# Kernel tuning notes

Hardware: AMD Instinct MI355X
Metric: run time of the kernel (lower is better)

## Reference

```python
import jax, jax.numpy as jnp
import numpy as np

NUM_C = 1000
DIM_S = 128
SIZE_M = 64
B = 64
L = 512


def setup_inputs() -> dict:
    key = jax.random.key(0)
    ks = jax.random.split(key, 16)
    d = DIM_S
    inp = {
        "q": jax.random.randint(ks[0], (B, L), 0, NUM_C),
        "r": jax.random.randint(ks[1], (B, L), 0, 2),
        # embeddings
        "Ek": jax.random.normal(ks[2], (NUM_C, d), jnp.float32),
        "Ev": jax.random.normal(ks[3], (2 * NUM_C, d), jnp.float32),
        # memory key / initial value memory (kaiming-normal-ish)
        "Mk": jax.random.normal(ks[4], (SIZE_M, d), jnp.float32) * np.sqrt(2.0 / d),
        "Mv0": jax.random.normal(ks[5], (SIZE_M, d), jnp.float32) * np.sqrt(2.0 / d),
        # erase / add layers (d -> d)
        "We": jax.random.normal(ks[6], (d, d), jnp.float32) / np.sqrt(d),
        "be": jnp.zeros((d,), jnp.float32),
        "Wa": jax.random.normal(ks[7], (d, d), jnp.float32) / np.sqrt(d),
        "ba": jnp.zeros((d,), jnp.float32),
        # f layer (2d -> d)
        "Wf": jax.random.normal(ks[8], (2 * d, d), jnp.float32) / np.sqrt(2 * d),
        "bf": jnp.zeros((d,), jnp.float32),
        # p layer (d -> 1)
        "Wp": jax.random.normal(ks[9], (d, 1), jnp.float32) / np.sqrt(d),
        "bp": jnp.zeros((1,), jnp.float32),
    }
    return inp


def reference(q, r, Ek, Ev, Mk, Mv0, We, be, Wa, ba, Wf, bf, Wp, bp):
    # q, r: [B, L] int
    x = q + NUM_C * r
    k = Ek[q]            # [B, L, D]  (k_original; no extra features when use_ed=use_mp=0)
    v = Ev[x]            # [B, L, D]

    # correlation weights over memory slots
    w = jax.nn.softmax(jnp.einsum("bld,md->blm", k, Mk), axis=-1)  # [B, L, M]

    e = jax.nn.sigmoid(v @ We + be)  # [B, L, D] erase
    a = jnp.tanh(v @ Wa + ba)        # [B, L, D] add

    def step(Mvt, inputs):
        wt, et, at = inputs            # [B,M], [B,D], [B,D]
        # read from memory BEFORE the update (matches Mv[:, :-1] in torch)
        read = jnp.einsum("bm,bmd->bd", wt, Mvt)
        Mvt_new = Mvt * (1.0 - wt[:, :, None] * et[:, None, :]) + wt[:, :, None] * at[:, None, :]
        return Mvt_new, read

    Mv_init = jnp.broadcast_to(Mv0[None], (q.shape[0], SIZE_M, DIM_S))
    xs = (jnp.swapaxes(w, 0, 1), jnp.swapaxes(e, 0, 1), jnp.swapaxes(a, 0, 1))
    _, reads = jax.lax.scan(step, Mv_init, xs)      # reads: [L, B, D]
    read_content = jnp.swapaxes(reads, 0, 1)        # [B, L, D]

    f = jnp.tanh(jnp.concatenate([read_content, k], axis=-1) @ Wf + bf)  # [B, L, D]
    # dropout in eval mode -> identity
    p = jax.nn.sigmoid(f @ Wp + bp)[..., 0]         # [B, L]
    return p
```

## Files before the change

### kernel.cpp

```cpp
#include <hip/hip_runtime.h>
#include <hip/hip_bf16.h>

#define NUM_C 1000
#define DIM   128
#define MM    64
#define BB    64
#define LL    512
#define NROWS (BB * LL)

typedef unsigned short u16;
typedef unsigned int   u32;
typedef short bfrag __attribute__((ext_vector_type(8)));
typedef float f32x4 __attribute__((ext_vector_type(4)));

__device__ __forceinline__ float sigmoidf_fast(float x) { return 1.f / (1.f + __expf(-x)); }
__device__ __forceinline__ float tanhf_fast(float x) { return 1.f - 2.f / (__expf(2.f * x) + 1.f); }

__device__ __forceinline__ u16 f2bf(float x) {
    u32 u = __float_as_uint(x);
    return (u16)((u + 0x7FFFu + ((u >> 16) & 1u)) >> 16);
}
__device__ __forceinline__ float bf2f(u16 h) { return __uint_as_float(((u32)h) << 16); }

__device__ __forceinline__ float quad_swap1(float x) {
    return __int_as_float(__builtin_amdgcn_mov_dpp(__float_as_int(x), 0xB1, 0xF, 0xF, true));
}
__device__ __forceinline__ float quad_swap2(float x) {
    return __int_as_float(__builtin_amdgcn_mov_dpp(__float_as_int(x), 0x4E, 0xF, 0xF, true));
}
__device__ __forceinline__ float row_ror4(float x) {
    return __int_as_float(__builtin_amdgcn_mov_dpp(__float_as_int(x), 0x124, 0xF, 0xF, true));
}
__device__ __forceinline__ float row_ror8(float x) {
    return __int_as_float(__builtin_amdgcn_mov_dpp(__float_as_int(x), 0x128, 0xF, 0xF, true));
}

__device__ __forceinline__ void ld16(const void* g, void* l) {
    __builtin_amdgcn_global_load_lds(
        (const __attribute__((address_space(1))) unsigned int*)g,
        (__attribute__((address_space(3))) unsigned int*)l, 16, 0, 0);
}

__global__ __launch_bounds__(256) void kP(const float* __restrict__ We,
                                          const float* __restrict__ Wa,
                                          const float* __restrict__ Wf,
                                          const float* __restrict__ Mk,
                                          const float* __restrict__ Ek,
                                          const float* __restrict__ Ev,
                                          u16* weT_hi, u16* weT_lo,
                                          u16* waT_hi, u16* waT_lo,
                                          u16* wfT_hi, u16* wfT_lo,
                                          u16* mkT_hi, u16* mkT_lo,
                                          u16* ekbf, u16* evbf) {
    int idx = blockIdx.x * 256 + threadIdx.x;
    if (idx < 128 * 128) {
        int n = idx >> 7, k = idx & 127;
        float we = We[k * DIM + n];
        u16 h = f2bf(we);
        weT_hi[idx] = h; weT_lo[idx] = f2bf(we - bf2f(h));
        float wa = Wa[k * DIM + n];
        u16 h2 = f2bf(wa);
        waT_hi[idx] = h2; waT_lo[idx] = f2bf(wa - bf2f(h2));
    }
    if (idx < 64 * 128) {
        float mk = Mk[idx];
        u16 h = f2bf(mk);
        mkT_hi[idx] = h; mkT_lo[idx] = f2bf(mk - bf2f(h));
    }
    {
        int n = idx >> 8, k = idx & 255;
        float wf = Wf[k * DIM + n];
        u16 h = f2bf(wf);
        wfT_hi[idx] = h; wfT_lo[idx] = f2bf(wf - bf2f(h));
    }
    for (int i = idx; i < NUM_C * DIM; i += 32768) ekbf[i] = f2bf(Ek[i]);
    for (int i = idx; i < 2 * NUM_C * DIM; i += 32768) evbf[i] = f2bf(Ev[i]);
}

__global__ __launch_bounds__(256) void kAB(const int* __restrict__ q,
                                           const int* __restrict__ r,
                                           const u16* __restrict__ ekbf,
                                           const u16* __restrict__ evbf,
                                           const u16* __restrict__ mkT_hi, const u16* __restrict__ mkT_lo,
                                           const u16* __restrict__ weT_hi, const u16* __restrict__ weT_lo,
                                           const u16* __restrict__ waT_hi, const u16* __restrict__ waT_lo,
                                           const float* __restrict__ be, const float* __restrict__ ba,
                                           float* __restrict__ w_out,
                                           float2* __restrict__ ea_out) {
    __shared__ __align__(16) u16 shi[4][16][136];
    __shared__ float slab[4][64];
    const int tid = threadIdx.x;
    const int lane = tid & 63;
    const int wv = tid >> 6;
    const int nloc = lane & 15;
    const int quad = lane >> 4;

    if (blockIdx.x < 512) {
        const int base = blockIdx.x * 64;
        {
            const int row_l = tid >> 2;
            const int rts = row_l >> 4, ms = row_l & 15;
            const int d0 = (tid & 3) * 32;
            const u16* src = ekbf + (size_t)q[base + row_l] * DIM + d0;
            #pragma unroll
            for (int c8 = 0; c8 < 4; ++c8)
                *reinterpret_cast<bfrag*>(&shi[rts][ms][d0 + c8 * 8]) =
                    *reinterpret_cast<const bfrag*>(src + c8 * 8);
        }
        __syncthreads();

        const int n = wv * 16 + nloc;
        bfrag Bh[4], Bl[4];
        #pragma unroll
        for (int kc = 0; kc < 4; ++kc) {
            const int ko = kc * 32 + quad * 8;
            Bh[kc] = *reinterpret_cast<const bfrag*>(mkT_hi + n * DIM + ko);
            Bl[kc] = *reinterpret_cast<const bfrag*>(mkT_lo + n * DIM + ko);
        }

        f32x4 acc[4];
        #pragma unroll
        for (int t = 0; t < 4; ++t) acc[t] = 0.f;

        #pragma unroll
        for (int rt = 0; rt < 4; ++rt) {
            #pragma unroll
            for (int kc = 0; kc < 4; ++kc) {
                const int ko = kc * 32 + quad * 8;
                bfrag Ah = *reinterpret_cast<const bfrag*>(&shi[rt][nloc][ko]);
                acc[rt] = __builtin_amdgcn_mfma_f32_16x16x32_bf16(Ah, Bh[kc], acc[rt], 0, 0, 0);
                acc[rt] = __builtin_amdgcn_mfma_f32_16x16x32_bf16(Ah, Bl[kc], acc[rt], 0, 0, 0);
            }
        }

        float ex[4][4];
        #pragma unroll
        for (int rt = 0; rt < 4; ++rt) {
            #pragma unroll
            for (int rg = 0; rg < 4; ++rg) {
                float e = __expf(acc[rt][rg]);
                ex[rt][rg] = e;
                float s = e;
                s += __shfl_xor(s, 1);
                s += __shfl_xor(s, 2);
                s += __shfl_xor(s, 4);
                s += __shfl_xor(s, 8);
                if (nloc == 0) slab[wv][rt * 16 + quad * 4 + rg] = s;
            }
        }
        __syncthreads();

        #pragma unroll
        for (int rt = 0; rt < 4; ++rt) {
            #pragma unroll
            for (int rg = 0; rg < 4; ++rg) {
                const int row = rt * 16 + quad * 4 + rg;
                float tot = slab[0][row] + slab[1][row] + slab[2][row] + slab[3][row];
                w_out[(size_t)(base + row) * MM + n] = ex[rt][rg] / tot;
            }
        }
    } else {
        const int base = (blockIdx.x - 512) * 64;
        {
            const int row_l = tid >> 2;
            const int rts = row_l >> 4, ms = row_l & 15;
            const int d0 = (tid & 3) * 32;
            const int row = base + row_l;
            const int x = q[row] + NUM_C * r[row];
            const u16* src = evbf + (size_t)x * DIM + d0;
            #pragma unroll
            for (int c8 = 0; c8 < 4; ++c8)
                *reinterpret_cast<bfrag*>(&shi[rts][ms][d0 + c8 * 8]) =
                    *reinterpret_cast<const bfrag*>(src + c8 * 8);
        }
        __syncthreads();

        #pragma unroll
        for (int dt = 0; dt < 2; ++dt) {
            const int n = (wv * 2 + dt) * 16 + nloc;
            bfrag Beh[4], Bel[4], Bah[4], Bal[4];
            #pragma unroll
            for (int kc = 0; kc < 4; ++kc) {
                const int ko = kc * 32 + quad * 8;
                Beh[kc] = *reinterpret_cast<const bfrag*>(weT_hi + n * DIM + ko);
                Bel[kc] = *reinterpret_cast<const bfrag*>(weT_lo + n * DIM + ko);
                Bah[kc] = *reinterpret_cast<const bfrag*>(waT_hi + n * DIM + ko);
                Bal[kc] = *reinterpret_cast<const bfrag*>(waT_lo + n * DIM + ko);
            }
            f32x4 acc_e[4], acc_a[4];
            #pragma unroll
            for (int t = 0; t < 4; ++t) { acc_e[t] = 0.f; acc_a[t] = 0.f; }

            #pragma unroll
            for (int rt = 0; rt < 4; ++rt) {
                #pragma unroll
                for (int kc = 0; kc < 4; ++kc) {
                    const int ko = kc * 32 + quad * 8;
                    bfrag Ah = *reinterpret_cast<const bfrag*>(&shi[rt][nloc][ko]);
                    acc_e[rt] = __builtin_amdgcn_mfma_f32_16x16x32_bf16(Ah, Beh[kc], acc_e[rt], 0, 0, 0);
                    acc_a[rt] = __builtin_amdgcn_mfma_f32_16x16x32_bf16(Ah, Bah[kc], acc_a[rt], 0, 0, 0);
                    acc_e[rt] = __builtin_amdgcn_mfma_f32_16x16x32_bf16(Ah, Bel[kc], acc_e[rt], 0, 0, 0);
                    acc_a[rt] = __builtin_amdgcn_mfma_f32_16x16x32_bf16(Ah, Bal[kc], acc_a[rt], 0, 0, 0);
                }
            }
            const float bev = be[n], bav = ba[n];
            #pragma unroll
            for (int rt = 0; rt < 4; ++rt) {
                #pragma unroll
                for (int rg = 0; rg < 4; ++rg) {
                    const int row = base + rt * 16 + quad * 4 + rg;
                    float2 ea;
                    ea.x = sigmoidf_fast(acc_e[rt][rg] + bev);
                    ea.y = tanhf_fast(acc_a[rt][rg] + bav);
                    ea_out[(size_t)row * DIM + n] = ea;
                }
            }
        }
    }
}

__device__ __forceinline__ void scan32(const float* wb, const float2* eab,
                                       int m0, int dl, int p, int t0,
                                       float (&Mv)[4], float* rp) {
    #pragma unroll
    for (int u = 0; u < 32; ++u) {
        float4 w4 = *reinterpret_cast<const float4*>(wb + u * 64 + m0);
        float2 ea = eab[u * 32 + dl];
        float wv[4] = {w4.x, w4.y, w4.z, w4.w};
        float e_c = ea.x, a_c = ea.y;
        float part = 0.f;
        #pragma unroll
        for (int j = 0; j < 4; ++j) {
            float old = Mv[j];
            part = fmaf(wv[j], old, part);
            Mv[j] = fmaf(wv[j], fmaf(-old, e_c, a_c), old);
        }
        part += quad_swap1(part);
        part += quad_swap2(part);
        part += row_ror4(part);
        part += row_ror8(part);
        if (p == 0) rp[(size_t)(t0 + u) * DIM] = part;
    }
}

__global__ __launch_bounds__(512) void kC(const float* __restrict__ Mv0,
                                          const float* __restrict__ w_in,
                                          const float2* __restrict__ ea_in,
                                          float* __restrict__ rd) {
    __shared__ __align__(16) float  wlds[2][32][64];
    __shared__ __align__(16) float2 ealds[2][32][32];
    const int tid = threadIdx.x;
    const int lane = tid & 63;
    const int wvid = tid >> 6;
    const int p = tid & 15;
    const int dl = tid >> 4;
    const int ds = blockIdx.x, b = blockIdx.y;
    const int d = ds * 32 + dl;
    const int m0 = p * 4;

    const char* wsrc  = (const char*)(w_in + (size_t)b * LL * MM);
    const char* easrc = (const char*)(ea_in + (size_t)b * LL * DIM + ds * 32);
    float* rp = rd + (size_t)b * LL * DIM + d;

    auto dma = [&](int c, int bufi) {
        const char* wt = wsrc + (size_t)c * 8192;
        char* wl = (char*)&wlds[bufi][0][0];
        char* el = (char*)&ealds[bufi][0][0];
        const int off = wvid * 1024 + lane * 16;
        ld16(wt + off, wl + off);
        const int tl = off >> 8, wi = off & 255;
        ld16(easrc + (size_t)(c * 32 + tl) * (DIM * 8) + wi, el + off);
    };

    dma(0, 0);

    float Mv[4];
    #pragma unroll
    for (int j = 0; j < 4; ++j)
        Mv[j] = Mv0[(m0 + j) * DIM + d];

    __builtin_amdgcn_s_waitcnt(0x0F70);
    __syncthreads();

    int buf = 0;
    for (int c = 0; c < LL / 32; ++c) {
        if (c + 1 < LL / 32) dma(c + 1, buf ^ 1);
        scan32(&wlds[buf][0][0], &ealds[buf][0][0], m0, dl, p, c * 32, Mv, rp);
        if (c + 1 < LL / 32) {
            __builtin_amdgcn_s_waitcnt(0x8F70);
            __syncthreads();
            buf ^= 1;
        }
    }
}

__global__ __launch_bounds__(256) void kD(const int* __restrict__ q,
                                          const u16* __restrict__ ekbf,
                                          const u16* __restrict__ wfT_hi, const u16* __restrict__ wfT_lo,
                                          const float* __restrict__ bfv,
                                          const float* __restrict__ Wp, const float* __restrict__ bp,
                                          const float* __restrict__ rd,
                                          float* __restrict__ out) {
    __shared__ __align__(16) u16 xhi[4][16][264];
    __shared__ float sred[64][4];
    const int tid = threadIdx.x;
    const int base = blockIdx.x * 64;
    const int row_l = tid >> 2;
    const int rts = row_l >> 4, ms = row_l & 15;
    const int d0 = (tid & 3) * 32;
    const int row = base + row_l;

    {
        const float* src = rd + (size_t)row * DIM + d0;
        #pragma unroll
        for (int c8 = 0; c8 < 4; ++c8) {
            float4 f0 = *reinterpret_cast<const float4*>(src + c8 * 8);
            float4 f1 = *reinterpret_cast<const float4*>(src + c8 * 8 + 4);
            float xs[8] = {f0.x, f0.y, f0.z, f0.w, f1.x, f1.y, f1.z, f1.w};
            bfrag h;
            #pragma unroll
            for (int j = 0; j < 8; ++j) h[j] = (short)f2bf(xs[j]);
            *reinterpret_cast<bfrag*>(&xhi[rts][ms][d0 + c8 * 8]) = h;
        }
    }
    {
        const u16* src = ekbf + (size_t)q[row] * DIM + d0;
        #pragma unroll
        for (int c8 = 0; c8 < 4; ++c8)
            *reinterpret_cast<bfrag*>(&xhi[rts][ms][128 + d0 + c8 * 8]) =
                *reinterpret_cast<const bfrag*>(src + c8 * 8);
    }
    __syncthreads();

    const int lane = tid & 63;
    const int wv = tid >> 6;
    const int nloc = lane & 15;
    const int quad = lane >> 4;
    float* fbuf = reinterpret_cast<float*>(&xhi[0][0][0]);

    f32x4 acc[2][4];
    #pragma unroll
    for (int dt = 0; dt < 2; ++dt)
        #pragma unroll
        for (int t = 0; t < 4; ++t) acc[dt][t] = 0.f;

    #pragma unroll
    for (int dt = 0; dt < 2; ++dt) {
        const int n = (wv * 2 + dt) * 16 + nloc;
        bfrag Bh[8], Bl[8];
        #pragma unroll
        for (int kc = 0; kc < 8; ++kc) {
            const int ko = kc * 32 + quad * 8;
            Bh[kc] = *reinterpret_cast<const bfrag*>(wfT_hi + n * 256 + ko);
            Bl[kc] = *reinterpret_cast<const bfrag*>(wfT_lo + n * 256 + ko);
        }
        #pragma unroll
        for (int rt = 0; rt < 4; ++rt) {
            #pragma unroll
            for (int kc = 0; kc < 8; ++kc) {
                const int ko = kc * 32 + quad * 8;
                bfrag Ah = *reinterpret_cast<const bfrag*>(&xhi[rt][nloc][ko]);
                acc[dt][rt] = __builtin_amdgcn_mfma_f32_16x16x32_bf16(Ah, Bh[kc], acc[dt][rt], 0, 0, 0);
                acc[dt][rt] = __builtin_amdgcn_mfma_f32_16x16x32_bf16(Ah, Bl[kc], acc[dt][rt], 0, 0, 0);
            }
        }
    }
    __syncthreads();

    #pragma unroll
    for (int dt = 0; dt < 2; ++dt) {
        const int n = (wv * 2 + dt) * 16 + nloc;
        const float bfn = bfv[n], wpn = Wp[n];
        #pragma unroll
        for (int rt = 0; rt < 4; ++rt)
            #pragma unroll
            for (int rg = 0; rg < 4; ++rg)
                fbuf[(rt * 16 + quad * 4 + rg) * 132 + n] = tanhf_fast(acc[dt][rt][rg] + bfn) * wpn;
    }
    __syncthreads();

    {
        float s = 0.f;
        const int c = tid & 3;
        #pragma unroll
        for (int k = 0; k < 32; ++k) s += fbuf[row_l * 132 + c * 32 + k];
        sred[row_l][c] = s;
    }
    __syncthreads();
    if (tid < 64)
        out[base + tid] = sigmoidf_fast(sred[tid][0] + sred[tid][1] + sred[tid][2] + sred[tid][3] + bp[0]);
}

extern "C" void kernel_launch(void* const* d_in, const int* in_sizes, int n_in,
                              void* d_out, int out_size, void* d_ws, size_t ws_size,
                              hipStream_t stream) {
    const int*   q   = (const int*)d_in[0];
    const int*   r   = (const int*)d_in[1];
    const float* Ek  = (const float*)d_in[2];
    const float* Ev  = (const float*)d_in[3];
    const float* Mk  = (const float*)d_in[4];
    const float* Mv0 = (const float*)d_in[5];
    const float* We  = (const float*)d_in[6];
    const float* be  = (const float*)d_in[7];
    const float* Wa  = (const float*)d_in[8];
    const float* ba  = (const float*)d_in[9];
    const float* Wf  = (const float*)d_in[10];
    const float* bfv = (const float*)d_in[11];
    const float* Wp  = (const float*)d_in[12];
    const float* bp  = (const float*)d_in[13];
    float* out = (float*)d_out;

    float*  ws     = (float*)d_ws;
    float*  w_buf  = ws;
    float2* ea_buf = (float2*)(w_buf + (size_t)NROWS * MM);
    float*  rd     = (float*)(ea_buf + (size_t)NROWS * DIM);

    u16* weT_hi = (u16*)(rd + (size_t)NROWS * DIM);
    u16* weT_lo = weT_hi + 16384;
    u16* waT_hi = weT_lo + 16384;
    u16* waT_lo = waT_hi + 16384;
    u16* wfT_hi = waT_lo + 16384;
    u16* wfT_lo = wfT_hi + 32768;
    u16* mkT_hi = wfT_lo + 32768;
    u16* mkT_lo = mkT_hi + 8192;
    u16* ekbf   = mkT_lo + 8192;
    u16* evbf   = ekbf + 128000;

    kP<<<dim3(128), 256, 0, stream>>>(We, Wa, Wf, Mk, Ek, Ev,
                                      weT_hi, weT_lo, waT_hi, waT_lo,
                                      wfT_hi, wfT_lo, mkT_hi, mkT_lo, ekbf, evbf);
    kAB<<<dim3(1024), 256, 0, stream>>>(q, r, ekbf, evbf, mkT_hi, mkT_lo,
                                        weT_hi, weT_lo, waT_hi, waT_lo,
                                        be, ba, w_buf, ea_buf);
    kC<<<dim3(4, BB), 512, 0, stream>>>(Mv0, w_buf, ea_buf, rd);
    kD<<<dim3(NROWS / 64), 256, 0, stream>>>(q, ekbf, wfT_hi, wfT_lo, bfv, Wp, bp, rd, out);
}
```

Baseline: 174.2 us.

## Replace LDS double-buffered scan with register prefetch queue of direct global loads

The recurrent memory-update kernel stops staging w and erase/add chunks through LDS with async global-to-LDS copies and barriers. Each thread now keeps an 8-deep rolling register queue of its own float4 weights and float2 erase/add values, loaded straight from global memory. The per-step dot product is split into two partial chains, and the grid is reordered so the batch is the fast block index. This removes the barriers and LDS round-trips, but relies on the cache absorbing redundant loads across the 32 d-lanes and may expose global latency if the prefetch depth is too shallow.

```diff
diff --git a/kernel.cpp b/kernel.cpp
--- a/kernel.cpp
+++ b/kernel.cpp
@@ -33,12 +33,6 @@
 }
 __device__ __forceinline__ float row_ror8(float x) {
     return __int_as_float(__builtin_amdgcn_mov_dpp(__float_as_int(x), 0x128, 0xF, 0xF, true));
-}
-
-__device__ __forceinline__ void ld16(const void* g, void* l) {
-    __builtin_amdgcn_global_load_lds(
-        (const __attribute__((address_space(1))) unsigned int*)g,
-        (__attribute__((address_space(3))) unsigned int*)l, 16, 0, 0);
 }
 
 __global__ __launch_bounds__(256) void kP(const float* __restrict__ We,
@@ -219,79 +213,73 @@
     }
 }
 
-__device__ __forceinline__ void scan32(const float* wb, const float2* eab,
-                                       int m0, int dl, int p, int t0,
-                                       float (&Mv)[4], float* rp) {
-    #pragma unroll
-    for (int u = 0; u < 32; ++u) {
-        float4 w4 = *reinterpret_cast<const float4*>(wb + u * 64 + m0);
-        float2 ea = eab[u * 32 + dl];
-        float wv[4] = {w4.x, w4.y, w4.z, w4.w};
-        float e_c = ea.x, a_c = ea.y;
-        float part = 0.f;
-        #pragma unroll
-        for (int j = 0; j < 4; ++j) {
-            float old = Mv[j];
-            part = fmaf(wv[j], old, part);
-            Mv[j] = fmaf(wv[j], fmaf(-old, e_c, a_c), old);
-        }
-        part += quad_swap1(part);
-        part += quad_swap2(part);
-        part += row_ror4(part);
-        part += row_ror8(part);
-        if (p == 0) rp[(size_t)(t0 + u) * DIM] = part;
-    }
-}
-
 __global__ __launch_bounds__(512) void kC(const float* __restrict__ Mv0,
                                           const float* __restrict__ w_in,
                                           const float2* __restrict__ ea_in,
                                           float* __restrict__ rd) {
-    __shared__ __align__(16) float  wlds[2][32][64];
-    __shared__ __align__(16) float2 ealds[2][32][32];
     const int tid = threadIdx.x;
-    const int lane = tid & 63;
-    const int wvid = tid >> 6;
-    const int p = tid & 15;
+    const int p  = tid & 15;
     const int dl = tid >> 4;
-    const int ds = blockIdx.x, b = blockIdx.y;
-    const int d = ds * 32 + dl;
+    const int b  = blockIdx.x;
+    const int ds = blockIdx.y;
+    const int d  = ds * 32 + dl;
     const int m0 = p * 4;
 
-    const char* wsrc  = (const char*)(w_in + (size_t)b * LL * MM);
-    const char* easrc = (const char*)(ea_in + (size_t)b * LL * DIM + ds * 32);
+    const float4* __restrict__ wsrc =
+        reinterpret_cast<const float4*>(w_in + (size_t)b * LL * MM) + p;
+    const float2* __restrict__ easrc = ea_in + (size_t)b * LL * DIM + d;
     float* rp = rd + (size_t)b * LL * DIM + d;
-
-    auto dma = [&](int c, int bufi) {
-        const char* wt = wsrc + (size_t)c * 8192;
-        char* wl = (char*)&wlds[bufi][0][0];
-        char* el = (char*)&ealds[bufi][0][0];
-        const int off = wvid * 1024 + lane * 16;
-        ld16(wt + off, wl + off);
-        const int tl = off >> 8, wi = off & 255;
-        ld16(easrc + (size_t)(c * 32 + tl) * (DIM * 8) + wi, el + off);
-    };
-
-    dma(0, 0);
 
     float Mv[4];
     #pragma unroll
     for (int j = 0; j < 4; ++j)
         Mv[j] = Mv0[(m0 + j) * DIM + d];
 
-    __builtin_amdgcn_s_waitcnt(0x0F70);
-    __syncthreads();
-
-    int buf = 0;
-    for (int c = 0; c < LL / 32; ++c) {
-        if (c + 1 < LL / 32) dma(c + 1, buf ^ 1);
-        scan32(&wlds[buf][0][0], &ealds[buf][0][0], m0, dl, p, c * 32, Mv, rp);
-        if (c + 1 < LL / 32) {
-            __builtin_amdgcn_s_waitcnt(0x8F70);
-            __syncthreads();
-            buf ^= 1;
-        }
-    }
+    constexpr int PF = 8;
+    float4 wq[PF];
+    float2 eq[PF];
+    #pragma unroll
+    for (int u = 0; u < PF; ++u) {
+        wq[u] = wsrc[u * 16];
+        eq[u] = easrc[(size_t)u * DIM];
+    }
+
+#define KC_STEP(W4, EA, T)                                                  \
+    {                                                                       \
+        float wv0 = (W4).x, wv1 = (W4).y, wv2 = (W4).z, wv3 = (W4).w;       \
+        float e_c = (EA).x, a_c = (EA).y;                                   \
+        float old0 = Mv[0], old1 = Mv[1], old2 = Mv[2], old3 = Mv[3];       \
+        float pp0 = wv0 * old0;                                             \
+        pp0 = fmaf(wv1, old1, pp0);                                         \
+        float pp1 = wv2 * old2;                                             \
+        pp1 = fmaf(wv3, old3, pp1);                                         \
+        Mv[0] = fmaf(wv0, fmaf(-old0, e_c, a_c), old0);                     \
+        Mv[1] = fmaf(wv1, fmaf(-old1, e_c, a_c), old1);                     \
+        Mv[2] = fmaf(wv2, fmaf(-old2, e_c, a_c), old2);                     \
+        Mv[3] = fmaf(wv3, fmaf(-old3, e_c, a_c), old3);                     \
+        float part = pp0 + pp1;                                             \
+        part += quad_swap1(part);                                           \
+        part += quad_swap2(part);                                           \
+        part += row_ror4(part);                                             \
+        part += row_ror8(part);                                             \
+        if (p == 0) rp[(size_t)(T) * DIM] = part;                           \
+    }
+
+    int t0 = 0;
+    for (; t0 < LL - PF; t0 += PF) {
+        #pragma unroll
+        for (int j = 0; j < PF; ++j) {
+            float4 w4 = wq[j];
+            float2 ea = eq[j];
+            wq[j] = wsrc[(t0 + PF + j) * 16];
+            eq[j] = easrc[(size_t)(t0 + PF + j) * DIM];
+            KC_STEP(w4, ea, t0 + j);
+        }
+    }
+    #pragma unroll
+    for (int j = 0; j < PF; ++j)
+        KC_STEP(wq[j], eq[j], t0 + j);
+#undef KC_STEP
 }
 
 __global__ __launch_bounds__(256) void kD(const int* __restrict__ q,
@@ -432,6 +420,6 @@
     kAB<<<dim3(1024), 256, 0, stream>>>(q, r, ekbf, evbf, mkT_hi, mkT_lo,
                                         weT_hi, weT_lo, waT_hi, waT_lo,
                                         be, ba, w_buf, ea_buf);
-    kC<<<dim3(4, BB), 512, 0, stream>>>(Mv0, w_buf, ea_buf, rd);
+    kC<<<dim3(BB, 4), 512, 0, stream>>>(Mv0, w_buf, ea_buf, rd);
     kD<<<dim3(NROWS / 64), 256, 0, stream>>>(q, ekbf, wfT_hi, wfT_lo, bfv, Wp, bp, rd, out);
 }
```

After: 196.5 us. 1.13x slower.

## Remap scan kernel so each wave covers all memory slots for four columns

Applied to the files above, without the earlier changes.

The recurrent memory-scan kernel now splits DIM into 16-column slices across 512 blocks of 256 threads, up from 256 blocks of 512. Each wave handles 4 columns across all 64 slots. Each lane loads one w scalar and exchanges it within its quad via DPP, using an XOR-permuted slot assignment. The per-step read reduction now spans the full wave with permlane16/32 swaps, and LDS loads are software-prefetched four steps ahead. The aim is more parallel blocks and cheaper LDS traffic on the serial scan, at the cost of a longer cross-lane reduction per step.

```diff
diff --git a/kernel.cpp b/kernel.cpp
--- a/kernel.cpp
+++ b/kernel.cpp
@@ -12,6 +12,7 @@
 typedef unsigned int   u32;
 typedef short bfrag __attribute__((ext_vector_type(8)));
 typedef float f32x4 __attribute__((ext_vector_type(4)));
+typedef unsigned uv2 __attribute__((ext_vector_type(2)));
 
 __device__ __forceinline__ float sigmoidf_fast(float x) { return 1.f / (1.f + __expf(-x)); }
 __device__ __forceinline__ float tanhf_fast(float x) { return 1.f - 2.f / (__expf(2.f * x) + 1.f); }
@@ -28,11 +29,31 @@
 __device__ __forceinline__ float quad_swap2(float x) {
     return __int_as_float(__builtin_amdgcn_mov_dpp(__float_as_int(x), 0x4E, 0xF, 0xF, true));
 }
+__device__ __forceinline__ float quad_rev(float x) {
+    return __int_as_float(__builtin_amdgcn_mov_dpp(__float_as_int(x), 0x1B, 0xF, 0xF, true));
+}
 __device__ __forceinline__ float row_ror4(float x) {
     return __int_as_float(__builtin_amdgcn_mov_dpp(__float_as_int(x), 0x124, 0xF, 0xF, true));
 }
 __device__ __forceinline__ float row_ror8(float x) {
     return __int_as_float(__builtin_amdgcn_mov_dpp(__float_as_int(x), 0x128, 0xF, 0xF, true));
+}
+
+__device__ __forceinline__ float xor16_sum(float x) {
+#if __has_builtin(__builtin_amdgcn_permlane16_swap)
+    uv2 r = __builtin_amdgcn_permlane16_swap(__float_as_uint(x), __float_as_uint(x), false, false);
+    return __uint_as_float(r.x) + __uint_as_float(r.y);
+#else
+    return x + __int_as_float(__builtin_amdgcn_ds_swizzle(__float_as_int(x), 0x401F));
+#endif
+}
+__device__ __forceinline__ float xor32_sum(float x) {
+#if __has_builtin(__builtin_amdgcn_permlane32_swap)
+    uv2 r = __builtin_amdgcn_permlane32_swap(__float_as_uint(x), __float_as_uint(x), false, false);
+    return __uint_as_float(r.x) + __uint_as_float(r.y);
+#else
+    return x + __shfl_xor(x, 32);
+#endif
 }
 
 __device__ __forceinline__ void ld16(const void* g, void* l) {
@@ -220,55 +241,76 @@
 }
 
 __device__ __forceinline__ void scan32(const float* wb, const float2* eab,
-                                       int m0, int dl, int p, int t0,
-                                       float (&Mv)[4], float* rp) {
+                                       int lane, int jcol, float (&Mv)[4],
+                                       float* rp, int t0, bool wr) {
+    constexpr int PF = 4;
+    float  wq[PF];
+    float2 eq[PF];
+    #pragma unroll
+    for (int u = 0; u < PF; ++u) {
+        wq[u] = wb[u * 64 + lane];
+        eq[u] = eab[u * 16 + jcol];
+    }
     #pragma unroll
     for (int u = 0; u < 32; ++u) {
-        float4 w4 = *reinterpret_cast<const float4*>(wb + u * 64 + m0);
-        float2 ea = eab[u * 32 + dl];
-        float wv[4] = {w4.x, w4.y, w4.z, w4.w};
+        float  x  = wq[u & 3];
+        float2 ea = eq[u & 3];
+        if (u + PF < 32) {
+            wq[u & 3] = wb[(u + PF) * 64 + lane];
+            eq[u & 3] = eab[(u + PF) * 16 + jcol];
+        }
+        float x1 = quad_swap1(x);
+        float x2 = quad_swap2(x);
+        float x3 = quad_rev(x);
         float e_c = ea.x, a_c = ea.y;
-        float part = 0.f;
-        #pragma unroll
-        for (int j = 0; j < 4; ++j) {
-            float old = Mv[j];
-            part = fmaf(wv[j], old, part);
-            Mv[j] = fmaf(wv[j], fmaf(-old, e_c, a_c), old);
-        }
-        part += quad_swap1(part);
-        part += quad_swap2(part);
+
+        float o0 = Mv[0], o1 = Mv[1], o2 = Mv[2], o3 = Mv[3];
+        float pp0 = x * o0;
+        pp0 = fmaf(x1, o1, pp0);
+        float pp1 = x2 * o2;
+        pp1 = fmaf(x3, o3, pp1);
+        Mv[0] = fmaf(x , fmaf(-o0, e_c, a_c), o0);
+        Mv[1] = fmaf(x1, fmaf(-o1, e_c, a_c), o1);
+        Mv[2] = fmaf(x2, fmaf(-o2, e_c, a_c), o2);
+        Mv[3] = fmaf(x3, fmaf(-o3, e_c, a_c), o3);
+        float part = pp0 + pp1;
+
         part += row_ror4(part);
         part += row_ror8(part);
-        if (p == 0) rp[(size_t)(t0 + u) * DIM] = part;
-    }
-}
-
-__global__ __launch_bounds__(512) void kC(const float* __restrict__ Mv0,
+        part = xor16_sum(part);
+        part = xor32_sum(part);
+        if (wr) rp[(size_t)(t0 + u) * DIM] = part;
+    }
+}
+
+__global__ __launch_bounds__(256) void kC(const float* __restrict__ Mv0,
                                           const float* __restrict__ w_in,
                                           const float2* __restrict__ ea_in,
                                           float* __restrict__ rd) {
     __shared__ __align__(16) float  wlds[2][32][64];
-    __shared__ __align__(16) float2 ealds[2][32][32];
-    const int tid = threadIdx.x;
+    __shared__ __align__(16) float2 ealds[2][32][16];
+    const int tid  = threadIdx.x;
     const int lane = tid & 63;
-    const int wvid = tid >> 6;
-    const int p = tid & 15;
-    const int dl = tid >> 4;
-    const int ds = blockIdx.x, b = blockIdx.y;
-    const int d = ds * 32 + dl;
-    const int m0 = p * 4;
+    const int wv   = tid >> 6;
+    const int p    = lane >> 2;
+    const int dl   = lane & 3;
+    const int b    = blockIdx.x;
+    const int ds   = blockIdx.y;
+    const int jcol = wv * 4 + dl;
+    const int d    = ds * 16 + jcol;
 
     const char* wsrc  = (const char*)(w_in + (size_t)b * LL * MM);
-    const char* easrc = (const char*)(ea_in + (size_t)b * LL * DIM + ds * 32);
+    const char* easrc = (const char*)(ea_in + (size_t)b * LL * DIM + ds * 16);
     float* rp = rd + (size_t)b * LL * DIM + d;
 
     auto dma = [&](int c, int bufi) {
         const char* wt = wsrc + (size_t)c * 8192;
         char* wl = (char*)&wlds[bufi][0][0];
         char* el = (char*)&ealds[bufi][0][0];
-        const int off = wvid * 1024 + lane * 16;
+        const int off = tid * 16;
         ld16(wt + off, wl + off);
-        const int tl = off >> 8, wi = off & 255;
+        ld16(wt + 4096 + off, wl + 4096 + off);
+        const int tl = tid >> 3, wi = (tid & 7) * 16;
         ld16(easrc + (size_t)(c * 32 + tl) * (DIM * 8) + wi, el + off);
     };
 
@@ -277,15 +319,16 @@
     float Mv[4];
     #pragma unroll
     for (int j = 0; j < 4; ++j)
-        Mv[j] = Mv0[(m0 + j) * DIM + d];
+        Mv[j] = Mv0[(size_t)(p * 4 + (dl ^ j)) * DIM + d];
 
     __builtin_amdgcn_s_waitcnt(0x0F70);
     __syncthreads();
 
+    const bool wr = (lane < 4);
     int buf = 0;
     for (int c = 0; c < LL / 32; ++c) {
         if (c + 1 < LL / 32) dma(c + 1, buf ^ 1);
-        scan32(&wlds[buf][0][0], &ealds[buf][0][0], m0, dl, p, c * 32, Mv, rp);
+        scan32(&wlds[buf][0][0], &ealds[buf][0][0], lane, jcol, Mv, rp, c * 32, wr);
         if (c + 1 < LL / 32) {
             __builtin_amdgcn_s_waitcnt(0x8F70);
             __syncthreads();
@@ -432,6 +475,6 @@
     kAB<<<dim3(1024), 256, 0, stream>>>(q, r, ekbf, evbf, mkT_hi, mkT_lo,
                                         weT_hi, weT_lo, waT_hi, waT_lo,
                                         be, ba, w_buf, ea_buf);
-    kC<<<dim3(4, BB), 512, 0, stream>>>(Mv0, w_buf, ea_buf, rd);
+    kC<<<dim3(BB, 8), 256, 0, stream>>>(Mv0, w_buf, ea_buf, rd);
     kD<<<dim3(NROWS / 64), 256, 0, stream>>>(q, ekbf, wfT_hi, wfT_lo, bfv, Wp, bp, rd, out);
 }
```

Result: slower. 181.0 us (+3.9%).

## Store softmax weights and erase/add intermediates as bf16 to halve scan traffic

Applied to the files above, without the earlier changes.

The attention weights and the packed erase/add values are now written as bf16 (the pair packed into one u32) instead of fp32, which halves the workspace traffic between the producer kernel and the sequential scan kernel. The scan kernel's LDS staging and async copies are resized to match, with half the threads loading weights and half loading erase/add. The scan loop also prefetches LDS values four steps ahead in registers and splits the read dot product into two chains. This lowers the precision of the recurrent memory update inputs, and rounding error can build up over the 512 steps.

```diff
diff --git a/kernel.cpp b/kernel.cpp
--- a/kernel.cpp
+++ b/kernel.cpp
@@ -85,8 +85,8 @@
                                            const u16* __restrict__ weT_hi, const u16* __restrict__ weT_lo,
                                            const u16* __restrict__ waT_hi, const u16* __restrict__ waT_lo,
                                            const float* __restrict__ be, const float* __restrict__ ba,
-                                           float* __restrict__ w_out,
-                                           float2* __restrict__ ea_out) {
+                                           u16* __restrict__ w_out,
+                                           u32* __restrict__ ea_out) {
     __shared__ __align__(16) u16 shi[4][16][136];
     __shared__ float slab[4][64];
     const int tid = threadIdx.x;
@@ -156,7 +156,7 @@
             for (int rg = 0; rg < 4; ++rg) {
                 const int row = rt * 16 + quad * 4 + rg;
                 float tot = slab[0][row] + slab[1][row] + slab[2][row] + slab[3][row];
-                w_out[(size_t)(base + row) * MM + n] = ex[rt][rg] / tot;
+                w_out[(size_t)(base + row) * MM + n] = f2bf(ex[rt][rg] / tot);
             }
         }
     } else {
@@ -209,32 +209,51 @@
                 #pragma unroll
                 for (int rg = 0; rg < 4; ++rg) {
                     const int row = base + rt * 16 + quad * 4 + rg;
-                    float2 ea;
-                    ea.x = sigmoidf_fast(acc_e[rt][rg] + bev);
-                    ea.y = tanhf_fast(acc_a[rt][rg] + bav);
-                    ea_out[(size_t)row * DIM + n] = ea;
+                    float ev = sigmoidf_fast(acc_e[rt][rg] + bev);
+                    float av = tanhf_fast(acc_a[rt][rg] + bav);
+                    ea_out[(size_t)row * DIM + n] = (u32)f2bf(ev) | ((u32)f2bf(av) << 16);
                 }
             }
         }
     }
 }
 
-__device__ __forceinline__ void scan32(const float* wb, const float2* eab,
+__device__ __forceinline__ void scan32(const u16* wb, const u32* eab,
                                        int m0, int dl, int p, int t0,
                                        float (&Mv)[4], float* rp) {
+    uint2 wq[4];
+    u32   eq[4];
+    #pragma unroll
+    for (int u = 0; u < 4; ++u) {
+        wq[u] = *reinterpret_cast<const uint2*>(wb + u * 64 + m0);
+        eq[u] = eab[u * 32 + dl];
+    }
     #pragma unroll
     for (int u = 0; u < 32; ++u) {
-        float4 w4 = *reinterpret_cast<const float4*>(wb + u * 64 + m0);
-        float2 ea = eab[u * 32 + dl];
-        float wv[4] = {w4.x, w4.y, w4.z, w4.w};
-        float e_c = ea.x, a_c = ea.y;
-        float part = 0.f;
-        #pragma unroll
-        for (int j = 0; j < 4; ++j) {
-            float old = Mv[j];
-            part = fmaf(wv[j], old, part);
-            Mv[j] = fmaf(wv[j], fmaf(-old, e_c, a_c), old);
-        }
+        uint2 wp = wq[u & 3];
+        u32   ep = eq[u & 3];
+        if (u + 4 < 32) {
+            wq[u & 3] = *reinterpret_cast<const uint2*>(wb + (u + 4) * 64 + m0);
+            eq[u & 3] = eab[(u + 4) * 32 + dl];
+        }
+        float wv0 = __uint_as_float(wp.x << 16);
+        float wv1 = __uint_as_float(wp.x & 0xffff0000u);
+        float wv2 = __uint_as_float(wp.y << 16);
+        float wv3 = __uint_as_float(wp.y & 0xffff0000u);
+        float e_c = __uint_as_float(ep << 16);
+        float a_c = __uint_as_float(ep & 0xffff0000u);
+
+        float o0 = Mv[0], o1 = Mv[1], o2 = Mv[2], o3 = Mv[3];
+        float pp0 = wv0 * o0;
+        pp0 = fmaf(wv1, o1, pp0);
+        float pp1 = wv2 * o2;
+        pp1 = fmaf(wv3, o3, pp1);
+        Mv[0] = fmaf(wv0, fmaf(-o0, e_c, a_c), o0);
+        Mv[1] = fmaf(wv1, fmaf(-o1, e_c, a_c), o1);
+        Mv[2] = fmaf(wv2, fmaf(-o2, e_c, a_c), o2);
+        Mv[3] = fmaf(wv3, fmaf(-o3, e_c, a_c), o3);
+        float part = pp0 + pp1;
+
         part += quad_swap1(part);
         part += quad_swap2(part);
         part += row_ror4(part);
@@ -244,14 +263,12 @@
 }
 
 __global__ __launch_bounds__(512) void kC(const float* __restrict__ Mv0,
-                                          const float* __restrict__ w_in,
-                                          const float2* __restrict__ ea_in,
+                                          const u16* __restrict__ w_in,
+                                          const u32* __restrict__ ea_in,
                                           float* __restrict__ rd) {
-    __shared__ __align__(16) float  wlds[2][32][64];
-    __shared__ __align__(16) float2 ealds[2][32][32];
+    __shared__ __align__(16) u16 wlds[2][32][64];
+    __shared__ __align__(16) u32 ealds[2][32][32];
     const int tid = threadIdx.x;
-    const int lane = tid & 63;
-    const int wvid = tid >> 6;
     const int p = tid & 15;
     const int dl = tid >> 4;
     const int ds = blockIdx.x, b = blockIdx.y;
@@ -263,13 +280,15 @@
     float* rp = rd + (size_t)b * LL * DIM + d;
 
     auto dma = [&](int c, int bufi) {
-        const char* wt = wsrc + (size_t)c * 8192;
-        char* wl = (char*)&wlds[bufi][0][0];
-        char* el = (char*)&ealds[bufi][0][0];
-        const int off = wvid * 1024 + lane * 16;
-        ld16(wt + off, wl + off);
-        const int tl = off >> 8, wi = off & 255;
-        ld16(easrc + (size_t)(c * 32 + tl) * (DIM * 8) + wi, el + off);
+        if (tid < 256) {
+            const char* wt = wsrc + (size_t)c * 4096;
+            ld16(wt + tid * 16, (char*)&wlds[bufi][0][0] + tid * 16);
+        } else {
+            const int idx = tid - 256;
+            const int tl = idx >> 3, wi = (idx & 7) * 16;
+            ld16(easrc + (size_t)(c * 32 + tl) * (DIM * 4) + wi,
+                 (char*)&ealds[bufi][0][0] + idx * 16);
+        }
     };
 
     dma(0, 0);
@@ -410,10 +429,9 @@
     const float* bp  = (const float*)d_in[13];
     float* out = (float*)d_out;
 
-    float*  ws     = (float*)d_ws;
-    float*  w_buf  = ws;
-    float2* ea_buf = (float2*)(w_buf + (size_t)NROWS * MM);
-    float*  rd     = (float*)(ea_buf + (size_t)NROWS * DIM);
+    u16*  w_buf  = (u16*)d_ws;
+    u32*  ea_buf = (u32*)(w_buf + (size_t)NROWS * MM);
+    float* rd    = (float*)(ea_buf + (size_t)NROWS * DIM);
 
     u16* weT_hi = (u16*)(rd + (size_t)NROWS * DIM);
     u16* weT_lo = weT_hi + 16384;
```

New measurement: 178.5 us. +2.5%, slower.
